# Kernel tuning notes

Hardware: AMD Instinct MI355X
Metric: run time of the kernel (lower is better)

Reference implementation:

```python
import jax, jax.numpy as jnp
import numpy as np

D_MODEL = 1024
NUM_HEADS = 16
OMEGA_0 = 30.0
D_K = D_MODEL // NUM_HEADS


def _siren_uniform(key, shape, fan_in, omega_0=OMEGA_0):
    bound = np.sqrt(6.0 / fan_in) / omega_0
    return jax.random.uniform(key, shape, minval=-bound, maxval=bound, dtype=jnp.float32)


def setup_inputs() -> dict:
    key = jax.random.key(0)
    ks = jax.random.split(key, 9)
    B, S = 2, 2048
    x = jax.random.normal(ks[0], (B, S, D_MODEL), dtype=jnp.float32)
    # weights stored as (out, in) like torch nn.Linear
    Wq = _siren_uniform(ks[1], (D_MODEL, D_MODEL), D_MODEL)
    bq = _siren_uniform(ks[2], (D_MODEL,), D_MODEL)
    Wk = _siren_uniform(ks[3], (D_MODEL, D_MODEL), D_MODEL)
    bk = _siren_uniform(ks[4], (D_MODEL,), D_MODEL)
    Wv = _siren_uniform(ks[5], (D_MODEL, D_MODEL), D_MODEL)
    bv = _siren_uniform(ks[6], (D_MODEL,), D_MODEL)
    Wo = _siren_uniform(ks[7], (D_MODEL, D_MODEL), D_MODEL)
    bo = _siren_uniform(ks[8], (D_MODEL,), D_MODEL)
    return {"x": x, "Wq": Wq, "bq": bq, "Wk": Wk, "bk": bk,
            "Wv": Wv, "bv": bv, "Wo": Wo, "bo": bo}


def reference(x, Wq, bq, Wk, bk, Wv, bv, Wo, bo):
    B, S, _ = x.shape
    scale = np.sqrt(D_K).astype(np.float32)
    # project and split heads: (B, H, S, d_k)
    def proj(W, b):
        y = jnp.einsum('bsd,ed->bse', x, W) + b
        return y.reshape(B, S, NUM_HEADS, D_K).transpose(0, 2, 1, 3)
    Q = proj(Wq, bq)
    K = proj(Wk, bk)
    V = proj(Wv, bv)
    logits = jnp.einsum('bhqd,bhkd->bhqk', Q, K) / scale
    attn = jnp.sin(OMEGA_0 * logits)  # no normalization
    out = jnp.einsum('bhqk,bhkd->bhqd', attn, V)
    out = out.transpose(0, 2, 1, 3).reshape(B, S, D_MODEL)
    return jnp.einsum('bsd,ed->bse', out, Wo) + bo
```

## Files before the change

kernel.cpp:

```cpp
#include <hip/hip_runtime.h>
#include <stdint.h>

typedef __attribute__((ext_vector_type(8))) __bf16 fragAB;
typedef __attribute__((ext_vector_type(4))) float f32x4;
typedef __attribute__((ext_vector_type(16))) float f32x16;
typedef __attribute__((ext_vector_type(4))) unsigned int u32x4;

__device__ __forceinline__ unsigned short f2bf(float f) {
    union { float f; unsigned int u; } v; v.f = f;
    unsigned int u = v.u + 0x7fffu + ((v.u >> 16) & 1u);
    return (unsigned short)(u >> 16);
}

__device__ __forceinline__ f32x4 MFMA16(fragAB a, fragAB b, f32x4 c) {
    return __builtin_amdgcn_mfma_f32_16x16x32_bf16(a, b, c, 0, 0, 0);
}
__device__ __forceinline__ f32x16 MFMA32(fragAB a, fragAB b, f32x16 c) {
    return __builtin_amdgcn_mfma_f32_32x32x16_bf16(a, b, c, 0, 0, 0);
}

__device__ __forceinline__ void gl16(const void* g, void* l) {
    __builtin_amdgcn_global_load_lds((const __attribute__((address_space(1))) void*)g,
                                     (__attribute__((address_space(3))) void*)l, 16, 0, 0);
}

__device__ __forceinline__ float fsin_rev(float rev) {
    float r; asm("v_sin_f32 %0, %1" : "=v"(r) : "v"(rev)); return r;
}
__device__ __forceinline__ unsigned int cvtpk(float lo, float hi) {
    unsigned int r; asm("v_cvt_pk_bf16_f32 %0, %1, %2" : "=v"(r) : "v"(lo), "v"(hi)); return r;
}
__device__ __forceinline__ void swap32(unsigned int& a, unsigned int& b) {
    asm volatile("v_permlane32_swap_b32 %0, %1" : "+v"(a), "+v"(b));
}

#define SIN_SC 0.5968310366f

__global__ __launch_bounds__(256) void cvt_all(
    const float* __restrict__ x,  const float* __restrict__ wq, const float* __restrict__ wk,
    const float* __restrict__ wv, const float* __restrict__ wo,
    unsigned short* __restrict__ xb,  unsigned short* __restrict__ wqb, unsigned short* __restrict__ wkb,
    unsigned short* __restrict__ wvb, unsigned short* __restrict__ wob)
{
    const int bid = blockIdx.x;
    const float* s; unsigned short* d; int off;
    if (bid < 4096)      { s = x;  d = xb;  off = bid; }
    else if (bid < 5120) { s = wq; d = wqb; off = bid - 4096; }
    else if (bid < 6144) { s = wk; d = wkb; off = bid - 5120; }
    else if (bid < 7168) { s = wv; d = wvb; off = bid - 6144; }
    else                 { s = wo; d = wob; off = bid - 7168; }
    const int i = (off * 256 + threadIdx.x) * 4;
    float4 f = *(const float4*)(s + i);
    ushort4 o;
    o.x = f2bf(f.x); o.y = f2bf(f.y); o.z = f2bf(f.z); o.w = f2bf(f.w);
    *(ushort4*)(d + i) = o;
}

__global__ __launch_bounds__(256, 2)
void gemm_k(const unsigned short* __restrict__ A,
            const unsigned short* __restrict__ W0, const unsigned short* __restrict__ W1,
            const unsigned short* __restrict__ W2,
            const float* __restrict__ b0, const float* __restrict__ b1, const float* __restrict__ b2,
            void* o0, void* o1, void* o2)
{
    __shared__ unsigned short As[8192];
    __shared__ unsigned short Ws[8192];

    const int z = blockIdx.z;
    const unsigned short* W = z == 0 ? W0 : (z == 1 ? W1 : W2);
    const float* bias        = z == 0 ? b0 : (z == 1 ? b1 : b2);
    void* out                = z == 0 ? o0 : (z == 1 ? o1 : o2);

    const int t = threadIdx.x;
    const int lane = t & 63;
    const int g = lane >> 4;
    const int c = lane & 15;
    const int w = t >> 6;
    const int wm = (w >> 1) * 64;
    const int wn = (w & 1) * 64;
    const int m0 = blockIdx.y * 128;
    const int n0 = blockIdx.x * 128;

    const int srow = lane >> 3;
    const int scol = (lane & 7) * 8;

    const f32x4 zz = {0.f, 0.f, 0.f, 0.f};
    f32x4 acc[4][4];
#pragma unroll
    for (int mi = 0; mi < 4; ++mi)
#pragma unroll
        for (int ni = 0; ni < 4; ++ni) acc[mi][ni] = zz;

    for (int kt = 0; kt < 16; ++kt) {
        const int k0 = kt * 64;
#pragma unroll
        for (int r = 0; r < 4; ++r) {
            gl16(A + (size_t)(m0 + 32 * w + 8 * r + srow) * 1024 + k0 + scol,
                 (unsigned short*)As + (w * 4 + r) * 512);
            gl16(W + (size_t)(n0 + 32 * w + 8 * r + srow) * 1024 + k0 + scol,
                 (unsigned short*)Ws + (w * 4 + r) * 512);
        }
        __syncthreads();
#pragma unroll
        for (int kk = 0; kk < 2; ++kk) {
            fragAB af[4], bfr[4];
#pragma unroll
            for (int mi = 0; mi < 4; ++mi)
                af[mi] = *(const fragAB*)((char*)As + (wm + mi * 16 + c) * 128 + kk * 64 + g * 16);
#pragma unroll
            for (int ni = 0; ni < 4; ++ni)
                bfr[ni] = *(const fragAB*)((char*)Ws + (wn + ni * 16 + c) * 128 + kk * 64 + g * 16);
#pragma unroll
            for (int mi = 0; mi < 4; ++mi)
#pragma unroll
                for (int ni = 0; ni < 4; ++ni)
                    acc[mi][ni] = MFMA16(af[mi], bfr[ni], acc[mi][ni]);
        }
        __syncthreads();
    }

    float bv[4];
#pragma unroll
    for (int ni = 0; ni < 4; ++ni) bv[ni] = bias[n0 + wn + ni * 16 + c];

    if (z == 0) {
        unsigned short* C = (unsigned short*)out;
#pragma unroll
        for (int mi = 0; mi < 4; ++mi)
#pragma unroll
            for (int ni = 0; ni < 4; ++ni)
#pragma unroll
                for (int j = 0; j < 4; ++j) {
                    const int grow = m0 + wm + mi * 16 + g * 4 + j;
                    const int gcol = n0 + wn + ni * 16 + c;
                    C[(size_t)grow * 1024 + gcol] = f2bf(acc[mi][ni][j] + bv[ni]);
                }
    } else if (z == 1) {
        unsigned short* Ksh = (unsigned short*)out;
#pragma unroll
        for (int mi = 0; mi < 4; ++mi) {
            const int s0 = m0 + wm + mi * 16 + g * 4;
            const int b_ = s0 >> 11, sr = s0 & 2047;
            const int kb = sr >> 6, kbl = (sr >> 5) & 1;
            const int l31b = (mi & 1) * 16 + g * 4;
#pragma unroll
            for (int ni = 0; ni < 4; ++ni) {
                const int n = n0 + wn + ni * 16 + c;
                const int h_ = n >> 6, d = n & 63;
                const int ds = d >> 4, e = d & 7, lhalf = (d >> 3) & 1;
                const size_t base =
                    ((((size_t)(b_ * 16 + h_) * 32 + kb) * 2 + kbl) * 4 + ds) * 512
                    + lhalf * 256 + (size_t)l31b * 8 + e;
#pragma unroll
                for (int j = 0; j < 4; ++j)
                    Ksh[base + j * 8] = f2bf(acc[mi][ni][j] + bv[ni]);
            }
        }
    } else {
        unsigned short* Vsh = (unsigned short*)out;
#pragma unroll
        for (int mi = 0; mi < 4; ++mi) {
            const int s0 = m0 + wm + mi * 16 + g * 4;
            const int b_ = s0 >> 11, sr = s0 & 2047;
            const int kb = sr >> 6;
            const int kslice = mi;
            const int khalf = (g >> 1) & 1;
            const int e0 = (g & 1) * 4;
#pragma unroll
            for (int ni = 0; ni < 4; ++ni) {
                const int n = n0 + wn + ni * 16 + c;
                const int h_ = n >> 6;
                const int nei = ni >> 1;
                const int l31 = (ni & 1) * 16 + c;
                const size_t base =
                    ((((size_t)(b_ * 16 + h_) * 32 + kb) * 4 + kslice) * 2 + nei) * 512
                    + (size_t)(khalf * 32 + l31) * 8 + e0;
                ushort4 pk;
                pk.x = f2bf(acc[mi][ni][0] + bv[ni]);
                pk.y = f2bf(acc[mi][ni][1] + bv[ni]);
                pk.z = f2bf(acc[mi][ni][2] + bv[ni]);
                pk.w = f2bf(acc[mi][ni][3] + bv[ni]);
                *(ushort4*)(Vsh + base) = pk;
            }
        }
    }
}

__global__ __launch_bounds__(256, 4)
void gemm64(const unsigned short* __restrict__ A,
            const unsigned short* __restrict__ W,
            const float* __restrict__ bias, float* __restrict__ out)
{
    __shared__ unsigned short As[4096];
    __shared__ unsigned short Ws[8192];

    const int t = threadIdx.x;
    const int lane = t & 63;
    const int g = lane >> 4;
    const int c = lane & 15;
    const int w = t >> 6;
    const int wm = (w >> 1) * 32;
    const int wn = (w & 1) * 64;
    const int m0 = blockIdx.y * 64;
    const int n0 = blockIdx.x * 128;

    const int srow = lane >> 3;
    const int scol = (lane & 7) * 8;

    const f32x4 zz = {0.f, 0.f, 0.f, 0.f};
    f32x4 acc[2][4];
#pragma unroll
    for (int mi = 0; mi < 2; ++mi)
#pragma unroll
        for (int ni = 0; ni < 4; ++ni) acc[mi][ni] = zz;

    for (int kt = 0; kt < 16; ++kt) {
        const int k0 = kt * 64;
        gl16(A + (size_t)(m0 + 16 * w + srow) * 1024 + k0 + scol,
             (unsigned short*)As + (2 * w) * 512);
        gl16(A + (size_t)(m0 + 16 * w + 8 + srow) * 1024 + k0 + scol,
             (unsigned short*)As + (2 * w + 1) * 512);
#pragma unroll
        for (int r = 0; r < 4; ++r)
            gl16(W + (size_t)(n0 + 32 * w + 8 * r + srow) * 1024 + k0 + scol,
                 (unsigned short*)Ws + (w * 4 + r) * 512);
        __syncthreads();
#pragma unroll
        for (int kk = 0; kk < 2; ++kk) {
            fragAB af[2], bfr[4];
#pragma unroll
            for (int mi = 0; mi < 2; ++mi)
                af[mi] = *(const fragAB*)((char*)As + (wm + mi * 16 + c) * 128 + kk * 64 + g * 16);
#pragma unroll
            for (int ni = 0; ni < 4; ++ni)
                bfr[ni] = *(const fragAB*)((char*)Ws + (wn + ni * 16 + c) * 128 + kk * 64 + g * 16);
#pragma unroll
            for (int mi = 0; mi < 2; ++mi)
#pragma unroll
                for (int ni = 0; ni < 4; ++ni)
                    acc[mi][ni] = MFMA16(af[mi], bfr[ni], acc[mi][ni]);
        }
        __syncthreads();
    }

#pragma unroll
    for (int ni = 0; ni < 4; ++ni) {
        const float bv = bias[n0 + wn + ni * 16 + c];
#pragma unroll
        for (int mi = 0; mi < 2; ++mi)
#pragma unroll
            for (int j = 0; j < 4; ++j) {
                const int grow = m0 + wm + mi * 16 + g * 4 + j;
                const int gcol = n0 + wn + ni * 16 + c;
                out[(size_t)grow * 1024 + gcol] = acc[mi][ni][j] + bv;
            }
    }
}

__global__ __launch_bounds__(256, 2)
void attn_kernel(const unsigned short* __restrict__ Qg,
                 const unsigned short* __restrict__ Ksh,
                 const unsigned short* __restrict__ Vsh,
                 unsigned short* __restrict__ AO)
{
    __shared__ char smem[32768];
    unsigned short* const KldsU = (unsigned short*)smem;
    unsigned short* const VldsU = (unsigned short*)(smem + 16384);
    float* const red = (float*)smem;

    const int t = threadIdx.x;
    const int lane = t & 63;
    const int l31 = lane & 31;
    const int lh = lane >> 5;
    const int w = t >> 6;
    const int qh = w >> 1;
    const int kbl = w & 1;

    const int bid = blockIdx.x;
    const int lb = (bid & 7) * 64 + (bid >> 3);
    const int qb = lb & 15;
    const int h = (lb >> 4) & 15;
    const int b = lb >> 8;
    const int qbase = qb * 128;

    const unsigned short* Kc = Ksh + (size_t)(b * 16 + h) * 131072;
    const unsigned short* Vc = Vsh + (size_t)(b * 16 + h) * 131072;

    fragAB qf[2][4];
#pragma unroll
    for (int qi = 0; qi < 2; ++qi)
#pragma unroll
        for (int ds = 0; ds < 4; ++ds)
            qf[qi][ds] = *(const fragAB*)(Qg
                + (size_t)(b * 2048 + qbase + qh * 64 + qi * 32 + l31) * 1024
                + h * 64 + ds * 16 + lh * 8);

    f32x16 o[2][2];
#pragma unroll
    for (int qi = 0; qi < 2; ++qi)
#pragma unroll
        for (int ni = 0; ni < 2; ++ni)
#pragma unroll
            for (int r = 0; r < 16; ++r) o[qi][ni][r] = 0.f;

    const int blk0 = 2 * w, blk1 = 2 * w + 1;

    gl16(Kc + blk0 * 512 + lane * 8, KldsU + blk0 * 512);
    gl16(Kc + blk1 * 512 + lane * 8, KldsU + blk1 * 512);
    gl16(Vc + blk0 * 512 + lane * 8, VldsU + blk0 * 512);
    gl16(Vc + blk1 * 512 + lane * 8, VldsU + blk1 * 512);
    __syncthreads();

    for (int kb = 0; kb < 32; ++kb) {
        const int buf = kb & 1;

        if (kb < 31) {
            const int nb = buf ^ 1;
            const size_t so = (size_t)(kb + 1) * 4096;
            gl16(Kc + so + blk0 * 512 + lane * 8, KldsU + nb * 4096 + blk0 * 512);
            gl16(Kc + so + blk1 * 512 + lane * 8, KldsU + nb * 4096 + blk1 * 512);
            gl16(Vc + so + blk0 * 512 + lane * 8, VldsU + nb * 4096 + blk0 * 512);
            gl16(Vc + so + blk1 * 512 + lane * 8, VldsU + nb * 4096 + blk1 * 512);
        }

        fragAB kf[4];
#pragma unroll
        for (int ds = 0; ds < 4; ++ds)
            kf[ds] = *(const fragAB*)(KldsU + buf * 4096 + (kbl * 4 + ds) * 512 + lane * 8);
        fragAB vf[2][2];
#pragma unroll
        for (int ks = 0; ks < 2; ++ks)
#pragma unroll
            for (int ni = 0; ni < 2; ++ni)
                vf[ks][ni] = *(const fragAB*)(VldsU + buf * 4096
                                              + ((kbl * 2 + ks) * 2 + ni) * 512 + lane * 8);

        f32x16 st[2];
#pragma unroll
        for (int qi = 0; qi < 2; ++qi)
#pragma unroll
            for (int r = 0; r < 16; ++r) st[qi][r] = 0.f;
        __builtin_amdgcn_s_setprio(1);
#pragma unroll
        for (int qi = 0; qi < 2; ++qi)
#pragma unroll
            for (int ds = 0; ds < 4; ++ds)
                st[qi] = MFMA32(kf[ds], qf[qi][ds], st[qi]);
        __builtin_amdgcn_s_setprio(0);

#pragma unroll
        for (int qi = 0; qi < 2; ++qi) {
            unsigned int u[8];
#pragma unroll
            for (int i = 0; i < 8; ++i)
                u[i] = cvtpk(fsin_rev(st[qi][2 * i] * SIN_SC),
                             fsin_rev(st[qi][2 * i + 1] * SIN_SC));
            swap32(u[0], u[2]); swap32(u[1], u[3]);
            swap32(u[4], u[6]); swap32(u[5], u[7]);
            union { u32x4 u; fragAB f; } pa0, pa1;
            pa0.u = (u32x4){u[0], u[1], u[2], u[3]};
            pa1.u = (u32x4){u[4], u[5], u[6], u[7]};
            __builtin_amdgcn_s_setprio(1);
#pragma unroll
            for (int ni = 0; ni < 2; ++ni) {
                o[qi][ni] = MFMA32(pa0.f, vf[0][ni], o[qi][ni]);
                o[qi][ni] = MFMA32(pa1.f, vf[1][ni], o[qi][ni]);
            }
            __builtin_amdgcn_s_setprio(0);
        }

        __syncthreads();
    }

    if (kbl) {
#pragma unroll
        for (int qi = 0; qi < 2; ++qi)
#pragma unroll
            for (int ni = 0; ni < 2; ++ni)
#pragma unroll
                for (int r = 0; r < 16; ++r)
                    red[(((qh * 2 + qi) * 2 + ni) * 16 + r) * 64 + lane] = o[qi][ni][r];
    }
    __syncthreads();
    if (!kbl) {
#pragma unroll
        for (int qi = 0; qi < 2; ++qi)
#pragma unroll
            for (int ni = 0; ni < 2; ++ni)
#pragma unroll
                for (int r = 0; r < 16; ++r) {
                    const float v = o[qi][ni][r]
                        + red[(((qh * 2 + qi) * 2 + ni) * 16 + r) * 64 + lane];
                    const int q = qbase + qh * 64 + qi * 32 + (r & 3) + 8 * (r >> 2) + 4 * lh;
                    AO[(size_t)(b * 2048 + q) * 1024 + h * 64 + ni * 32 + l31] = f2bf(v);
                }
    }
}

extern "C" void kernel_launch(void* const* d_in, const int* in_sizes, int n_in,
                              void* d_out, int out_size, void* d_ws, size_t ws_size,
                              hipStream_t stream) {
    (void)in_sizes; (void)n_in; (void)out_size; (void)ws_size;
    const float* x  = (const float*)d_in[0];
    const float* Wq = (const float*)d_in[1];
    const float* bq = (const float*)d_in[2];
    const float* Wk = (const float*)d_in[3];
    const float* bk = (const float*)d_in[4];
    const float* Wv = (const float*)d_in[5];
    const float* bv = (const float*)d_in[6];
    const float* Wo = (const float*)d_in[7];
    const float* bo = (const float*)d_in[8];

    char* ws = (char*)d_ws;
    unsigned short* xb    = (unsigned short*)(ws);
    unsigned short* Wqb   = (unsigned short*)(ws + (8u  << 20));
    unsigned short* Wkb   = (unsigned short*)(ws + (10u << 20));
    unsigned short* Wvb   = (unsigned short*)(ws + (12u << 20));
    unsigned short* Wob   = (unsigned short*)(ws + (14u << 20));
    unsigned short* Qb    = (unsigned short*)(ws + (16u << 20));
    unsigned short* Kshuf = (unsigned short*)(ws + (24u << 20));
    unsigned short* Vshuf = (unsigned short*)(ws + (32u << 20));
    unsigned short* AO    = (unsigned short*)(ws + (40u << 20));

    cvt_all<<<8192, 256, 0, stream>>>(x, Wq, Wk, Wv, Wo, xb, Wqb, Wkb, Wvb, Wob);

    gemm_k<<<dim3(8, 32, 3), 256, 0, stream>>>(xb, Wqb, Wkb, Wvb, bq, bk, bv,
                                               Qb, Kshuf, Vshuf);

    attn_kernel<<<512, 256, 0, stream>>>(Qb, Kshuf, Vshuf, AO);

    gemm64<<<dim3(8, 64), 256, 0, stream>>>(AO, Wob, bo, (float*)d_out);
}
```

Measured before the change: 106.8 us.

## Split attention work across eight waves with 32 queries per wave

Doubles the attention block to 512 threads so each wave handles one 32-query tile instead of two. K/V tile loads are spread across all eight waves, and the final cross-wave reduction is resized to match. The aim is more waves in flight to hide latency in the sin and MFMA pipeline. In exchange, each K/V fragment read from LDS now feeds half as many MFMAs. The launch bound of (512, 4) also sets a tight register budget that may cause spills.

```diff
diff --git a/kernel.cpp b/kernel.cpp
--- a/kernel.cpp
+++ b/kernel.cpp
@@ -257,7 +257,7 @@
     }
 }
 
-__global__ __launch_bounds__(256, 2)
+__global__ __launch_bounds__(512, 4)
 void attn_kernel(const unsigned short* __restrict__ Qg,
                  const unsigned short* __restrict__ Ksh,
                  const unsigned short* __restrict__ Vsh,
@@ -286,29 +286,21 @@
     const unsigned short* Kc = Ksh + (size_t)(b * 16 + h) * 131072;
     const unsigned short* Vc = Vsh + (size_t)(b * 16 + h) * 131072;
 
-    fragAB qf[2][4];
-#pragma unroll
-    for (int qi = 0; qi < 2; ++qi)
-#pragma unroll
-        for (int ds = 0; ds < 4; ++ds)
-            qf[qi][ds] = *(const fragAB*)(Qg
-                + (size_t)(b * 2048 + qbase + qh * 64 + qi * 32 + l31) * 1024
-                + h * 64 + ds * 16 + lh * 8);
-
-    f32x16 o[2][2];
-#pragma unroll
-    for (int qi = 0; qi < 2; ++qi)
-#pragma unroll
-        for (int ni = 0; ni < 2; ++ni)
-#pragma unroll
-            for (int r = 0; r < 16; ++r) o[qi][ni][r] = 0.f;
-
-    const int blk0 = 2 * w, blk1 = 2 * w + 1;
-
-    gl16(Kc + blk0 * 512 + lane * 8, KldsU + blk0 * 512);
-    gl16(Kc + blk1 * 512 + lane * 8, KldsU + blk1 * 512);
-    gl16(Vc + blk0 * 512 + lane * 8, VldsU + blk0 * 512);
-    gl16(Vc + blk1 * 512 + lane * 8, VldsU + blk1 * 512);
+    fragAB qf[4];
+#pragma unroll
+    for (int ds = 0; ds < 4; ++ds)
+        qf[ds] = *(const fragAB*)(Qg
+            + (size_t)(b * 2048 + qbase + qh * 32 + l31) * 1024
+            + h * 64 + ds * 16 + lh * 8);
+
+    f32x16 o[2];
+#pragma unroll
+    for (int ni = 0; ni < 2; ++ni)
+#pragma unroll
+        for (int r = 0; r < 16; ++r) o[ni][r] = 0.f;
+
+    gl16(Kc + w * 512 + lane * 8, KldsU + w * 512);
+    gl16(Vc + w * 512 + lane * 8, VldsU + w * 512);
     __syncthreads();
 
     for (int kb = 0; kb < 32; ++kb) {
@@ -317,10 +309,8 @@
         if (kb < 31) {
             const int nb = buf ^ 1;
             const size_t so = (size_t)(kb + 1) * 4096;
-            gl16(Kc + so + blk0 * 512 + lane * 8, KldsU + nb * 4096 + blk0 * 512);
-            gl16(Kc + so + blk1 * 512 + lane * 8, KldsU + nb * 4096 + blk1 * 512);
-            gl16(Vc + so + blk0 * 512 + lane * 8, VldsU + nb * 4096 + blk0 * 512);
-            gl16(Vc + so + blk1 * 512 + lane * 8, VldsU + nb * 4096 + blk1 * 512);
+            gl16(Kc + so + w * 512 + lane * 8, KldsU + nb * 4096 + w * 512);
+            gl16(Vc + so + w * 512 + lane * 8, VldsU + nb * 4096 + w * 512);
         }
 
         fragAB kf[4];
@@ -335,65 +325,54 @@
                 vf[ks][ni] = *(const fragAB*)(VldsU + buf * 4096
                                               + ((kbl * 2 + ks) * 2 + ni) * 512 + lane * 8);
 
-        f32x16 st[2];
-#pragma unroll
-        for (int qi = 0; qi < 2; ++qi)
-#pragma unroll
-            for (int r = 0; r < 16; ++r) st[qi][r] = 0.f;
+        f32x16 st;
+#pragma unroll
+        for (int r = 0; r < 16; ++r) st[r] = 0.f;
         __builtin_amdgcn_s_setprio(1);
 #pragma unroll
-        for (int qi = 0; qi < 2; ++qi)
-#pragma unroll
-            for (int ds = 0; ds < 4; ++ds)
-                st[qi] = MFMA32(kf[ds], qf[qi][ds], st[qi]);
+        for (int ds = 0; ds < 4; ++ds)
+            st = MFMA32(kf[ds], qf[ds], st);
         __builtin_amdgcn_s_setprio(0);
 
-#pragma unroll
-        for (int qi = 0; qi < 2; ++qi) {
-            unsigned int u[8];
-#pragma unroll
-            for (int i = 0; i < 8; ++i)
-                u[i] = cvtpk(fsin_rev(st[qi][2 * i] * SIN_SC),
-                             fsin_rev(st[qi][2 * i + 1] * SIN_SC));
-            swap32(u[0], u[2]); swap32(u[1], u[3]);
-            swap32(u[4], u[6]); swap32(u[5], u[7]);
-            union { u32x4 u; fragAB f; } pa0, pa1;
-            pa0.u = (u32x4){u[0], u[1], u[2], u[3]};
-            pa1.u = (u32x4){u[4], u[5], u[6], u[7]};
-            __builtin_amdgcn_s_setprio(1);
-#pragma unroll
-            for (int ni = 0; ni < 2; ++ni) {
-                o[qi][ni] = MFMA32(pa0.f, vf[0][ni], o[qi][ni]);
-                o[qi][ni] = MFMA32(pa1.f, vf[1][ni], o[qi][ni]);
-            }
-            __builtin_amdgcn_s_setprio(0);
-        }
+        unsigned int u[8];
+#pragma unroll
+        for (int i = 0; i < 8; ++i)
+            u[i] = cvtpk(fsin_rev(st[2 * i] * SIN_SC), fsin_rev(st[2 * i + 1] * SIN_SC));
+        swap32(u[0], u[2]); swap32(u[1], u[3]);
+        swap32(u[4], u[6]); swap32(u[5], u[7]);
+        union { u32x4 u; fragAB f; } pa0, pa1;
+        pa0.u = (u32x4){u[0], u[1], u[2], u[3]};
+        pa1.u = (u32x4){u[4], u[5], u[6], u[7]};
+
+        __builtin_amdgcn_s_setprio(1);
+#pragma unroll
+        for (int ni = 0; ni < 2; ++ni) {
+            o[ni] = MFMA32(pa0.f, vf[0][ni], o[ni]);
+            o[ni] = MFMA32(pa1.f, vf[1][ni], o[ni]);
+        }
+        __builtin_amdgcn_s_setprio(0);
 
         __syncthreads();
     }
 
     if (kbl) {
 #pragma unroll
-        for (int qi = 0; qi < 2; ++qi)
-#pragma unroll
-            for (int ni = 0; ni < 2; ++ni)
-#pragma unroll
-                for (int r = 0; r < 16; ++r)
-                    red[(((qh * 2 + qi) * 2 + ni) * 16 + r) * 64 + lane] = o[qi][ni][r];
+        for (int ni = 0; ni < 2; ++ni)
+#pragma unroll
+            for (int r = 0; r < 16; ++r)
+                red[((qh * 2 + ni) * 16 + r) * 64 + lane] = o[ni][r];
     }
     __syncthreads();
     if (!kbl) {
 #pragma unroll
-        for (int qi = 0; qi < 2; ++qi)
-#pragma unroll
-            for (int ni = 0; ni < 2; ++ni)
-#pragma unroll
-                for (int r = 0; r < 16; ++r) {
-                    const float v = o[qi][ni][r]
-                        + red[(((qh * 2 + qi) * 2 + ni) * 16 + r) * 64 + lane];
-                    const int q = qbase + qh * 64 + qi * 32 + (r & 3) + 8 * (r >> 2) + 4 * lh;
-                    AO[(size_t)(b * 2048 + q) * 1024 + h * 64 + ni * 32 + l31] = f2bf(v);
-                }
+        for (int ni = 0; ni < 2; ++ni)
+#pragma unroll
+            for (int r = 0; r < 16; ++r) {
+                const float v = o[ni][r]
+                    + red[((qh * 2 + ni) * 16 + r) * 64 + lane];
+                const int q = qbase + qh * 32 + (r & 3) + 8 * (r >> 2) + 4 * lh;
+                AO[(size_t)(b * 2048 + q) * 1024 + h * 64 + ni * 32 + l31] = f2bf(v);
+            }
     }
 }
 
@@ -427,7 +406,7 @@
     gemm_k<<<dim3(8, 32, 3), 256, 0, stream>>>(xb, Wqb, Wkb, Wvb, bq, bk, bv,
                                                Qb, Kshuf, Vshuf);
 
-    attn_kernel<<<512, 256, 0, stream>>>(Qb, Kshuf, Vshuf, AO);
+    attn_kernel<<<512, 512, 0, stream>>>(Qb, Kshuf, Vshuf, AO);
 
     gemm64<<<dim3(8, 64), 256, 0, stream>>>(AO, Wob, bo, (float*)d_out);
 }
```

Result: faster. 104.6 us (-2.0%).

## Load K/V fragments straight to registers and drop LDS staging in attention

Applied to the files above, without the earlier changes.

The attention kernel no longer stages K/V tiles in LDS with global_load_lds double buffering and a per-iteration __syncthreads. Each wave now reads its K and V MFMA fragments directly from global memory into registers, ping-ponging between two register sets to prefetch the next key block. Blocks are enlarged to 512 threads covering 256 queries, which halves the grid and lets more query waves reuse the same K/V lines through cache. The trade-off is redundant global and L2 traffic, since waves with the same kbl load identical fragments. Extra fragment registers under launch_bounds(512,2) also raise the risk of register spills or lower occupancy.

```diff
diff --git a/kernel.cpp b/kernel.cpp
--- a/kernel.cpp
+++ b/kernel.cpp
@@ -257,16 +257,13 @@
     }
 }
 
-__global__ __launch_bounds__(256, 2)
+__global__ __launch_bounds__(512, 2)
 void attn_kernel(const unsigned short* __restrict__ Qg,
                  const unsigned short* __restrict__ Ksh,
                  const unsigned short* __restrict__ Vsh,
                  unsigned short* __restrict__ AO)
 {
-    __shared__ char smem[32768];
-    unsigned short* const KldsU = (unsigned short*)smem;
-    unsigned short* const VldsU = (unsigned short*)(smem + 16384);
-    float* const red = (float*)smem;
+    __shared__ float red[16384];
 
     const int t = threadIdx.x;
     const int lane = t & 63;
@@ -277,14 +274,17 @@
     const int kbl = w & 1;
 
     const int bid = blockIdx.x;
-    const int lb = (bid & 7) * 64 + (bid >> 3);
-    const int qb = lb & 15;
-    const int h = (lb >> 4) & 15;
-    const int b = lb >> 8;
-    const int qbase = qb * 128;
+    const int lb = (bid & 7) * 32 + (bid >> 3);
+    const int qb = lb & 7;
+    const int h = (lb >> 3) & 15;
+    const int b = lb >> 7;
+    const int qbase = qb * 256;
 
     const unsigned short* Kc = Ksh + (size_t)(b * 16 + h) * 131072;
     const unsigned short* Vc = Vsh + (size_t)(b * 16 + h) * 131072;
+
+    const unsigned short* Kw = Kc + (size_t)kbl * 2048 + lane * 8;
+    const unsigned short* Vw = Vc + (size_t)kbl * 2048 + lane * 8;
 
     fragAB qf[2][4];
 #pragma unroll
@@ -303,37 +303,21 @@
 #pragma unroll
             for (int r = 0; r < 16; ++r) o[qi][ni][r] = 0.f;
 
-    const int blk0 = 2 * w, blk1 = 2 * w + 1;
-
-    gl16(Kc + blk0 * 512 + lane * 8, KldsU + blk0 * 512);
-    gl16(Kc + blk1 * 512 + lane * 8, KldsU + blk1 * 512);
-    gl16(Vc + blk0 * 512 + lane * 8, VldsU + blk0 * 512);
-    gl16(Vc + blk1 * 512 + lane * 8, VldsU + blk1 * 512);
-    __syncthreads();
-
-    for (int kb = 0; kb < 32; ++kb) {
-        const int buf = kb & 1;
-
+    fragAB kfA[4], vfA[4], kfB[4], vfB[4];
+#pragma unroll
+    for (int ds = 0; ds < 4; ++ds) kfA[ds] = *(const fragAB*)(Kw + ds * 512);
+#pragma unroll
+    for (int j = 0; j < 4; ++j)    vfA[j]  = *(const fragAB*)(Vw + j * 512);
+
+    auto body = [&](int kb, fragAB (&kfc)[4], fragAB (&vfc)[4],
+                            fragAB (&kfn)[4], fragAB (&vfn)[4]) {
         if (kb < 31) {
-            const int nb = buf ^ 1;
             const size_t so = (size_t)(kb + 1) * 4096;
-            gl16(Kc + so + blk0 * 512 + lane * 8, KldsU + nb * 4096 + blk0 * 512);
-            gl16(Kc + so + blk1 * 512 + lane * 8, KldsU + nb * 4096 + blk1 * 512);
-            gl16(Vc + so + blk0 * 512 + lane * 8, VldsU + nb * 4096 + blk0 * 512);
-            gl16(Vc + so + blk1 * 512 + lane * 8, VldsU + nb * 4096 + blk1 * 512);
-        }
-
-        fragAB kf[4];
-#pragma unroll
-        for (int ds = 0; ds < 4; ++ds)
-            kf[ds] = *(const fragAB*)(KldsU + buf * 4096 + (kbl * 4 + ds) * 512 + lane * 8);
-        fragAB vf[2][2];
-#pragma unroll
-        for (int ks = 0; ks < 2; ++ks)
-#pragma unroll
-            for (int ni = 0; ni < 2; ++ni)
-                vf[ks][ni] = *(const fragAB*)(VldsU + buf * 4096
-                                              + ((kbl * 2 + ks) * 2 + ni) * 512 + lane * 8);
+#pragma unroll
+            for (int ds = 0; ds < 4; ++ds) kfn[ds] = *(const fragAB*)(Kw + so + ds * 512);
+#pragma unroll
+            for (int j = 0; j < 4; ++j)    vfn[j]  = *(const fragAB*)(Vw + so + j * 512);
+        }
 
         f32x16 st[2];
 #pragma unroll
@@ -345,7 +329,7 @@
         for (int qi = 0; qi < 2; ++qi)
 #pragma unroll
             for (int ds = 0; ds < 4; ++ds)
-                st[qi] = MFMA32(kf[ds], qf[qi][ds], st[qi]);
+                st[qi] = MFMA32(kfc[ds], qf[qi][ds], st[qi]);
         __builtin_amdgcn_s_setprio(0);
 
 #pragma unroll
@@ -363,13 +347,16 @@
             __builtin_amdgcn_s_setprio(1);
 #pragma unroll
             for (int ni = 0; ni < 2; ++ni) {
-                o[qi][ni] = MFMA32(pa0.f, vf[0][ni], o[qi][ni]);
-                o[qi][ni] = MFMA32(pa1.f, vf[1][ni], o[qi][ni]);
+                o[qi][ni] = MFMA32(pa0.f, vfc[ni], o[qi][ni]);
+                o[qi][ni] = MFMA32(pa1.f, vfc[2 + ni], o[qi][ni]);
             }
             __builtin_amdgcn_s_setprio(0);
         }
-
-        __syncthreads();
+    };
+
+    for (int tt = 0; tt < 16; ++tt) {
+        body(2 * tt,     kfA, vfA, kfB, vfB);
+        body(2 * tt + 1, kfB, vfB, kfA, vfA);
     }
 
     if (kbl) {
@@ -427,7 +414,7 @@
     gemm_k<<<dim3(8, 32, 3), 256, 0, stream>>>(xb, Wqb, Wkb, Wvb, bq, bk, bv,
                                                Qb, Kshuf, Vshuf);
 
-    attn_kernel<<<512, 256, 0, stream>>>(Qb, Kshuf, Vshuf, AO);
+    attn_kernel<<<256, 512, 0, stream>>>(Qb, Kshuf, Vshuf, AO);
 
     gemm64<<<dim3(8, 64), 256, 0, stream>>>(AO, Wob, bo, (float*)d_out);
 }
```

Measured after the change: 104.1 us (median of 2 runs). -2.5%, faster.
